# Performance work log

Measured on AMD Instinct MI355X. Metric: run time of the kernel, lower is better.

The kernel has to match this reference:

```python
import jax, jax.numpy as jnp
import numpy as np

HIDDEN = 64
EF_DIM = 3
RBOUND = 10.0
GROUP = 5
NEXP_MEAN = 0.05   # fixed normalization constants of the 'nexpnorm' RBF
NEXP_STD = 0.15
COORDS_WEIGHT = 1.0
N_NODES = 100000
N_GRAPHS = N_NODES // GROUP


def act(x):
    return jax.nn.relu(x)


def rbf(dist, num_rbf):
    # ExpNormal smearing with cosine cutoff (non-trainable), then fixed normalization.
    # dist: (..., 1) -> (..., num_rbf)
    alpha = 5.0 / RBOUND
    start = float(np.exp(-RBOUND))
    means = jnp.linspace(start, 1.0, num_rbf).astype(dist.dtype)
    beta = (2.0 / num_rbf * (1.0 - start)) ** -2
    cutoff = 0.5 * (jnp.cos(dist * jnp.pi / RBOUND) + 1.0) * (dist <= RBOUND)
    r = cutoff * jnp.exp(-beta * (jnp.exp(-alpha * dist) - means) ** 2)
    return (r - NEXP_MEAN) / NEXP_STD


def safe_pdist(a, b):
    # pairwise L2 norm (B,G,1,3)-(B,1,G,3) -> (B,G,G,1); grad-safe at zero
    d = a[:, :, None, :] - b[:, None, :, :]
    sq = jnp.sum(d * d, axis=-1, keepdims=True)
    return jnp.sqrt(jnp.where(sq == 0.0, 1.0, sq)) * (sq > 0.0)


def mlp2(x, w1, b1, w2, b2):
    return act(act(x @ w1 + b1) @ w2 + b2)


def mixed_wl(row, col, coord, vel, ic_wef, ic_pat, br_w1, br_b1, br_w2, br_b2, out_w, out_b):
    B = coord.shape[0] // GROUP
    c = coord.reshape(B, GROUP, 3)
    v = vel.reshape(B, GROUP, 3)
    mcd = safe_pdist(c, v)  # mixed coord-vel distances
    ef = jnp.concatenate([
        rbf(safe_pdist(c, c), EF_DIM),
        rbf(safe_pdist(v, v), EF_DIM),
        rbf(mcd, EF_DIM),
        rbf(jnp.swapaxes(mcd, 1, 2), EF_DIM),
    ], axis=-1)  # (B, 5, 5, 4*EF_DIM)
    # TwoFDisInit: linear embed * pattern embedding (diag tuples get pattern id 2, off-diag 1)
    idx = jnp.arange(GROUP)
    pattern = jnp.ones((GROUP, GROUP), dtype=jnp.int32).at[idx, idx].set(2)
    kemb = (ef @ ic_wef) * ic_pat[pattern]  # (B, 5, 5, H)
    # TwoFDisLayer (color_steps = 1): three branch MLPs, matrix-multiply mixing, residual add
    sm = mlp2(kemb, br_w1[0], br_b1[0], br_w2[0], br_b2[0])
    k0 = mlp2(kemb, br_w1[1], br_b1[1], br_w2[1], br_b2[1])
    k1 = mlp2(kemb, br_w1[2], br_b1[2], br_w2[2], br_b2[2])
    mult = jnp.einsum('bijd,bjkd->bikd', k0, k1)
    kemb = kemb + act((sm * mult) @ out_w + out_b)
    # gather per-edge tuple embedding
    return kemb[row // GROUP, row % GROUP, col % GROUP]  # (E, H)


def setup_inputs():
    key = jax.random.key(0)
    ks = jax.random.split(key, 20)
    N, H = N_NODES, HIDDEN
    # fully-connected (no self loops) edges inside each 5-node graph
    pairs = np.array([(i, j) for i in range(GROUP) for j in range(GROUP) if i != j])
    off = np.arange(N_GRAPHS) * GROUP
    row = (off[:, None] + pairs[None, :, 0]).reshape(-1)
    col = (off[:, None] + pairs[None, :, 1]).reshape(-1)
    edge_index = jnp.asarray(np.stack([row, col]), dtype=jnp.int32)
    g = lambda k, shp, s=0.05: jax.random.normal(k, shp, dtype=jnp.float32) * s
    return {
        'h': g(ks[0], (N, H), 0.5),
        'coord': g(ks[1], (N, 3), 1.0),
        'vel': g(ks[2], (N, 3), 1.0),
        'edge_index': edge_index,
        'e_w1': g(ks[3], (2 * H + 1 + H, H)), 'e_b1': jnp.zeros((H,), jnp.float32),
        'e_w2': g(ks[4], (H, H)), 'e_b2': jnp.zeros((H,), jnp.float32),
        'n_w1': g(ks[5], (2 * H, H)), 'n_b1': jnp.zeros((H,), jnp.float32),
        'n_w2': g(ks[6], (H, H)), 'n_b2': jnp.zeros((H,), jnp.float32),
        'c_w1': g(ks[7], (H, H)), 'c_b1': jnp.zeros((H,), jnp.float32),
        'c_w2': g(ks[8], (H, 1), 0.001),  # xavier gain=0.001, bias-free
        'v_w1': g(ks[9], (H, H)), 'v_b1': jnp.zeros((H,), jnp.float32),
        'v_w2': g(ks[10], (H, 1)), 'v_b2': jnp.zeros((1,), jnp.float32),
        'ic_wef': g(ks[11], (4 * EF_DIM, H), 0.1),
        'ic_pat': g(ks[12], (3, H), 0.1),
        'br_w1': g(ks[13], (3, H, H)), 'br_b1': jnp.zeros((3, H), jnp.float32),
        'br_w2': g(ks[14], (3, H, H)), 'br_b2': jnp.zeros((3, H), jnp.float32),
        'out_w': g(ks[15], (H, H)), 'out_b': jnp.zeros((H,), jnp.float32),
    }


def reference(h, coord, vel, edge_index, e_w1, e_b1, e_w2, e_b2, n_w1, n_b1, n_w2, n_b2,
              c_w1, c_b1, c_w2, v_w1, v_b1, v_w2, v_b2, ic_wef, ic_pat,
              br_w1, br_b1, br_w2, br_b2, out_w, out_b):
    row, col = edge_index[0], edge_index[1]
    N = h.shape[0]
    # coord2radial (norm_diff=False)
    coord_diff = coord[row] - coord[col]                      # (E, 3)
    radial = jnp.sum(coord_diff * coord_diff, axis=1, keepdims=True)  # (E, 1)
    # mixed 2-WL tuple embedding per edge
    kemb = mixed_wl(row, col, coord, vel, ic_wef, ic_pat, br_w1, br_b1, br_w2, br_b2, out_w, out_b)
    # edge model (attention=False)
    edge_feat = mlp2(jnp.concatenate([h[row], h[col], radial, kemb], axis=1),
                     e_w1, e_b1, e_w2, e_b2)                  # (E, H)
    # coord model: per-edge scalar (num_vectors_in=out=1), clamp, segment mean
    cmat = act(edge_feat @ c_w1 + c_b1) @ c_w2                # (E, 1)
    trans = jnp.clip(coord_diff * cmat, -100.0, 100.0)        # (E, 3)
    cnt = jax.ops.segment_sum(jnp.ones((row.shape[0],), trans.dtype), row, num_segments=N)
    agg = jax.ops.segment_sum(trans, row, num_segments=N) / jnp.maximum(cnt, 1.0)[:, None]
    # velocity update: coord += coord_mlp_vel(h) * vel
    vmat = act(h @ v_w1 + v_b1) @ v_w2 + v_b2                 # (N, 1)
    coord_out = (coord + agg * COORDS_WEIGHT + vel * vmat)[:, :, None]  # (N, 3, 1)
    # node model (recurrent=True)
    nagg = jax.ops.segment_sum(edge_feat, row, num_segments=N)
    h_out = h + (act(jnp.concatenate([h, nagg], axis=1) @ n_w1 + n_b1) @ n_w2 + n_b2)
    return h_out, coord_out
```

## Files before the change

### kernel.cpp

```cpp
#include <hip/hip_runtime.h>
#include <math.h>

#define HD 64
#define WPB 2

typedef unsigned short u16;
typedef unsigned int u32;
typedef __attribute__((ext_vector_type(8))) short short8;
typedef __attribute__((ext_vector_type(4))) float f32x4;

__device__ __forceinline__ u16 f2bf(float f) {
  u32 r;
  asm("v_cvt_pk_bf16_f32 %0, %1, %2" : "=v"(r) : "v"(f), "v"(f));
  return (u16)r;
}
__device__ __forceinline__ u32 pk2(float lo, float hi) {
  u32 r;
  asm("v_cvt_pk_bf16_f32 %0, %1, %2" : "=v"(r) : "v"(lo), "v"(hi));
  return r;
}
__device__ __forceinline__ float bf2f(u16 x) {
  return __uint_as_float(((u32)x) << 16);
}
__device__ __forceinline__ int uswz(int row, int col) {
  return (row << 6) | (col ^ (((row >> 2) & 3) << 4));
}
__device__ __forceinline__ float rlane(float v, int l) {
  return __uint_as_float(__builtin_amdgcn_readlane(__float_as_uint(v), l));
}
__device__ __forceinline__ void fence() {
  asm volatile("s_waitcnt lgkmcnt(0)" ::: "memory");
}

template <int MT, int RMAX>
__device__ __forceinline__ void loadA(const u16* A_, int t, short8* a0, short8* a1) {
  const int q8 = (t >> 4) << 3;
#pragma unroll
  for (int mt = 0; mt < MT; ++mt) {
    int row = mt * 16 + (t & 15);
    row = row > RMAX ? RMAX : row;
    const int idx = uswz(row, q8);
    a0[mt] = *reinterpret_cast<const short8*>(A_ + idx);
    a1[mt] = *reinterpret_cast<const short8*>(A_ + (idx ^ 32));
  }
}

template <int MTT>
__device__ __forceinline__ void mmh(const short8* a0, const short8* a1,
                                    const u16* __restrict__ WT, f32x4 (*acc)[2],
                                    int t, int nh) {
  const int c15 = t & 15;
  const int q8 = (t >> 4) << 3;
  short8 b[2][2];
#pragma unroll
  for (int n2 = 0; n2 < 2; ++n2) {
    const int nt = nh * 2 + n2;
#pragma unroll
    for (int s = 0; s < 2; ++s)
      b[n2][s] = *reinterpret_cast<const short8*>(WT + (nt * 16 + c15) * 64 + s * 32 + q8);
  }
#pragma unroll
  for (int mt = 0; mt < MTT; ++mt) {
#pragma unroll
    for (int n2 = 0; n2 < 2; ++n2)
      acc[mt][n2] = __builtin_amdgcn_mfma_f32_16x16x32_bf16(a0[mt], b[n2][0], acc[mt][n2], 0, 0, 0);
#pragma unroll
    for (int n2 = 0; n2 < 2; ++n2)
      acc[mt][n2] = __builtin_amdgcn_mfma_f32_16x16x32_bf16(a1[mt], b[n2][1], acc[mt][n2], 0, 0, 0);
  }
}

template <int MT, int RMAX, int EPI>
__device__ __forceinline__ void run_phase2(const u16* AA, const u16* AB,
                                           u16* DA, u16* DB,
                                           const u16* MA, const u16* MB,
                                           const u16* __restrict__ WT,
                                           const float* __restrict__ bias,
                                           const u16* __restrict__ PF,
                                           u32& pfa, int t, int rowoff = 0) {
  const int c15 = t & 15, q = t >> 4;
  constexpr int rowlim = (MT == 2) ? 25 : 5;
  const u32 pfv = reinterpret_cast<const u32*>(PF)[t * 32];
  short8 a0[2 * MT], a1[2 * MT];
  loadA<MT, RMAX>(AA, t, a0, a1);
  loadA<MT, RMAX>(AB, t, a0 + MT, a1 + MT);
#pragma unroll
  for (int nh = 0; nh < 2; ++nh) {
    f32x4 acc[2 * MT][2];
#pragma unroll
    for (int n2 = 0; n2 < 2; ++n2) {
      const int col = (nh * 2 + n2) * 16 + c15;
      const float bb = bias ? bias[col] : 0.0f;
#pragma unroll
      for (int mt = 0; mt < 2 * MT; ++mt) acc[mt][n2] = (f32x4){bb, bb, bb, bb};
    }
    mmh<2 * MT>(a0, a1, WT, acc, t, nh);
#pragma unroll
    for (int n2 = 0; n2 < 2; ++n2) {
      const int col = (nh * 2 + n2) * 16 + c15;
#pragma unroll
      for (int mt = 0; mt < 2 * MT; ++mt) {
        u16* D_ = (mt < MT) ? DA : DB;
        const u16* M_ = (mt < MT) ? MA : MB;
        const int r0 = (mt % MT) * 16 + q * 4;
        const int bix = uswz(r0 + rowoff, col);
#pragma unroll
        for (int i = 0; i < 4; ++i) {
          if (r0 + i < rowlim) {
            const int ix = bix + i * 64;
            float v = acc[mt][n2][i];
            if (EPI >= 2) v = fmaxf(v, 0.0f);
            if (EPI == 3) v *= bf2f(M_[ix]);
            if (EPI == 4) v += bf2f(D_[ix]);
            D_[ix] = f2bf(v);
          }
        }
      }
    }
  }
  pfa ^= pfv;
}

__global__ __launch_bounds__(256) void prepack(
    const float* __restrict__ br_w1, const float* __restrict__ br_w2,
    const float* __restrict__ out_w, const float* __restrict__ e_w1,
    const float* __restrict__ e_w2, const float* __restrict__ c_w1,
    const float* __restrict__ v_w1, const float* __restrict__ n_w1,
    const float* __restrict__ n_w2, const float* __restrict__ ic_wef,
    u16* __restrict__ W) {
  const int m = blockIdx.x;
  if (m == 16) {
    for (int e = threadIdx.x; e < 2048; e += blockDim.x) {
      const int n = e >> 5, k = e & 31;
      W[16 * 4096 + e] = (k < 12) ? f2bf(ic_wef[k * 64 + n]) : (u16)0;
    }
    return;
  }
  const float* src;
  switch (m) {
    case 0: src = br_w1; break;
    case 1: src = br_w1 + 4096; break;
    case 2: src = br_w1 + 8192; break;
    case 3: src = br_w2; break;
    case 4: src = br_w2 + 4096; break;
    case 5: src = br_w2 + 8192; break;
    case 6: src = out_w; break;
    case 7: src = e_w1; break;
    case 8: src = e_w1 + 64 * 64; break;
    case 9: src = e_w1 + 129 * 64; break;
    case 10: src = e_w2; break;
    case 11: src = c_w1; break;
    case 12: src = v_w1; break;
    case 13: src = n_w1; break;
    case 14: src = n_w1 + 64 * 64; break;
    default: src = n_w2; break;
  }
  u16* dst = W + m * 4096;
  for (int e = threadIdx.x; e < 4096; e += blockDim.x) {
    const int n = e >> 6, k = e & 63;
    dst[e] = f2bf(src[k * 64 + n]);
  }
}

__global__ __launch_bounds__(64 * WPB, 2) void egcl_mfma(
    const float* __restrict__ gh, const float* __restrict__ gcoord,
    const float* __restrict__ gvel, const u16* __restrict__ Wg,
    const float* __restrict__ e_w1, const float* __restrict__ e_b1,
    const float* __restrict__ e_b2,
    const float* __restrict__ n_b1, const float* __restrict__ n_b2,
    const float* __restrict__ c_b1, const float* __restrict__ c_w2,
    const float* __restrict__ v_b1, const float* __restrict__ v_w2,
    const float* __restrict__ v_b2,
    const float* __restrict__ ic_pat,
    const float* __restrict__ br_b1, const float* __restrict__ br_b2,
    const float* __restrict__ out_b,
    float* __restrict__ hout, float* __restrict__ cout, int B) {
  __shared__ __align__(16) u16 arena[WPB][9600];

  const int t = threadIdx.x & 63;
  const int wv = threadIdx.x >> 6;
  const int gA = (blockIdx.x * WPB + wv) * 2;
  if (gA >= B) return;
  int gB = gA + 1;
  if (gB >= B) gB = gA;

  u16* AR = arena[wv];
  u16* KA = AR;           u16* KB = AR + 1600;
  u16* TA = AR + 3200;    u16* TB = AR + 4800;
  u16* UA = AR + 6400;    u16* UB = AR + 8000;
  u16* EFa = TA;
  u16* EFb = TB;
  const int c15 = t & 15, q = t >> 4, q8 = q << 3;
  u32 pfa = 0;
#define WT(m) (Wg + (m) * 4096)

  short8 hA0, hA1;
  {
    int nd = c15 & 7;
    nd = nd > 4 ? 4 : nd;
    const int gg = (c15 & 8) ? gB : gA;
    const float* hp = gh + (size_t)(gg * 5 + nd) * HD + q8;
    const float4 f0 = *reinterpret_cast<const float4*>(hp);
    const float4 f1 = *reinterpret_cast<const float4*>(hp + 4);
    const float4 f2 = *reinterpret_cast<const float4*>(hp + 32);
    const float4 f3 = *reinterpret_cast<const float4*>(hp + 36);
    union { u32 w[4]; short8 s; } u0, u1;
    u0.w[0] = pk2(f0.x, f0.y); u0.w[1] = pk2(f0.z, f0.w);
    u0.w[2] = pk2(f1.x, f1.y); u0.w[3] = pk2(f1.z, f1.w);
    u1.w[0] = pk2(f2.x, f2.y); u1.w[1] = pk2(f2.z, f2.w);
    u1.w[2] = pk2(f3.x, f3.y); u1.w[3] = pk2(f3.z, f3.w);
    hA0 = u0.s;
    hA1 = u1.s;
  }

  float scvreg = 0.0f;
  if (t < 15) scvreg = gcoord[gA * 15 + t];
  else if (t >= 16 && t < 31) scvreg = gvel[gA * 15 + (t - 16)];
  else if (t >= 32 && t < 47) scvreg = gcoord[gB * 15 + (t - 32)];
  else if (t >= 48 && t < 63) scvreg = gvel[gB * 15 + (t - 48)];

#pragma unroll
  for (int z = 0; z < 8; ++z) {
    const int e = t + z * 64;
    if (e < 500) {
      const int gsel = e >= 250;
      const int ee = e - gsel * 250;
      const int row = ee / 10, cc = 12 + (ee % 10) * 2;
      *reinterpret_cast<u32*>((gsel ? EFb : EFa) + row * 32 + cc) = 0u;
    }
  }

  float sqcc = 0.0f;
  {
    const int lb = (t >= 32) ? 32 : 0;
    const int tt = t - lb;
    if (tt < 25) {
      u16* EF = lb ? EFb : EFa;
      const int ti = tt / 5, tj = tt % 5;
      const float cix = __shfl(scvreg, lb + ti * 3 + 0, 64), ciy = __shfl(scvreg, lb + ti * 3 + 1, 64), ciz = __shfl(scvreg, lb + ti * 3 + 2, 64);
      const float cjx = __shfl(scvreg, lb + tj * 3 + 0, 64), cjy = __shfl(scvreg, lb + tj * 3 + 1, 64), cjz = __shfl(scvreg, lb + tj * 3 + 2, 64);
      const float vix = __shfl(scvreg, lb + 16 + ti * 3 + 0, 64), viy = __shfl(scvreg, lb + 16 + ti * 3 + 1, 64), viz = __shfl(scvreg, lb + 16 + ti * 3 + 2, 64);
      const float vjx = __shfl(scvreg, lb + 16 + tj * 3 + 0, 64), vjy = __shfl(scvreg, lb + 16 + tj * 3 + 1, 64), vjz = __shfl(scvreg, lb + 16 + tj * 3 + 2, 64);
      {
        const float dx = cix - cjx, dy = ciy - cjy, dz = ciz - cjz;
        sqcc = dx * dx + dy * dy + dz * dz;
      }
      auto sd = [](float sq) { return (sq > 0.0f) ? sqrtf(sq) : 0.0f; };
      float sq2;
      const float dcc = sd(sqcc);
      {
        const float dx = vix - vjx, dy = viy - vjy, dz = viz - vjz;
        sq2 = dx * dx + dy * dy + dz * dz;
      }
      const float dvv = sd(sq2);
      {
        const float dx = cix - vjx, dy = ciy - vjy, dz = ciz - vjz;
        sq2 = dx * dx + dy * dy + dz * dz;
      }
      const float dcv = sd(sq2);
      {
        const float dx = cjx - vix, dy = cjy - viy, dz = cjz - viz;
        sq2 = dx * dx + dy * dy + dz * dz;
      }
      const float dvc = sd(sq2);
      auto rbf3 = [&](float d, int base) {
        const float cut = (d <= 10.0f) ? (0.5f * (cosf(d * 0.31415926535897931f) + 1.0f)) : 0.0f;
        const float e = expf(-0.5f * d);
        const float u0 = e - 4.5399929762484854e-05f;
        const float u1 = e - 0.50002270f;
        const float u2 = e - 1.0f;
        const float BETA = 2.2502043f;
        EF[tt * 32 + base + 0] = f2bf((cut * expf(-BETA * u0 * u0) - 0.05f) * (1.0f / 0.15f));
        EF[tt * 32 + base + 1] = f2bf((cut * expf(-BETA * u1 * u1) - 0.05f) * (1.0f / 0.15f));
        EF[tt * 32 + base + 2] = f2bf((cut * expf(-BETA * u2 * u2) - 0.05f) * (1.0f / 0.15f));
      };
      rbf3(dcc, 0);
      rbf3(dvv, 3);
      rbf3(dcv, 6);
      rbf3(dvc, 9);
    }
  }
  fence();

  {
    const u32 pfv = reinterpret_cast<const u32*>(WT(1))[t * 32];
    short8 aE[4];
#pragma unroll
    for (int gsel = 0; gsel < 2; ++gsel) {
      const u16* EF = gsel ? EFb : EFa;
#pragma unroll
      for (int mt = 0; mt < 2; ++mt) {
        int row = mt * 16 + c15;
        row = row > 24 ? 24 : row;
        aE[gsel * 2 + mt] = *reinterpret_cast<const short8*>(EF + row * 32 + q8);
      }
    }
    const u16* WTp = Wg + 16 * 4096;
#pragma unroll
    for (int nh = 0; nh < 2; ++nh) {
      f32x4 acc[4][2];
#pragma unroll
      for (int mt = 0; mt < 4; ++mt)
#pragma unroll
        for (int n2 = 0; n2 < 2; ++n2) acc[mt][n2] = (f32x4){0.f, 0.f, 0.f, 0.f};
      short8 b[2];
#pragma unroll
      for (int n2 = 0; n2 < 2; ++n2)
        b[n2] = *reinterpret_cast<const short8*>(WTp + ((nh * 2 + n2) * 16 + c15) * 32 + q8);
#pragma unroll
      for (int mt = 0; mt < 4; ++mt)
#pragma unroll
        for (int n2 = 0; n2 < 2; ++n2)
          acc[mt][n2] = __builtin_amdgcn_mfma_f32_16x16x32_bf16(aE[mt], b[n2], acc[mt][n2], 0, 0, 0);
#pragma unroll
      for (int n2 = 0; n2 < 2; ++n2) {
        const int col = (nh * 2 + n2) * 16 + c15;
        const float p1 = ic_pat[64 + col], p2 = ic_pat[128 + col];
#pragma unroll
        for (int mt = 0; mt < 4; ++mt) {
          u16* K_ = (mt < 2) ? KA : KB;
          const int r0 = (mt & 1) * 16 + q * 4;
          const int bix = uswz(r0, col);
#pragma unroll
          for (int i = 0; i < 4; ++i) {
            const int row = r0 + i;
            if (row < 25) {
              const bool diag = (row % 6) == 0;
              K_[bix + i * 64] = f2bf(acc[mt][n2][i] * (diag ? p2 : p1));
            }
          }
        }
      }
    }
    pfa ^= pfv;
  }
  fence();

  float svc[4][4];

  run_phase2<2, 24, 2>(KA, KB, TA, TB, nullptr, nullptr, WT(1), br_b1 + 64, WT(4), pfa, t); fence();
  run_phase2<2, 24, 2>(TA, TB, UA, UB, nullptr, nullptr, WT(4), br_b2 + 64, WT(2), pfa, t); fence();
  run_phase2<2, 24, 2>(KA, KB, TA, TB, nullptr, nullptr, WT(2), br_b1 + 128, WT(5), pfa, t); fence();
  run_phase2<2, 24, 2>(TA, TB, TA, TB, nullptr, nullptr, WT(5), br_b2 + 128, WT(0), pfa, t); fence();

  {
    float mu[2][25];
#pragma unroll
    for (int gsel = 0; gsel < 2; ++gsel)
#pragma unroll
      for (int p = 0; p < 25; ++p) mu[gsel][p] = 0.0f;
#pragma unroll
    for (int j = 0; j < 5; ++j) {
#pragma unroll
      for (int gsel = 0; gsel < 2; ++gsel) {
        const u16* Tg = gsel ? TB : TA;
        const u16* Ug = gsel ? UB : UA;
        float k1r[5], k0c[5];
#pragma unroll
        for (int k = 0; k < 5; ++k) k1r[k] = bf2f(Tg[uswz(j * 5 + k, t)]);
#pragma unroll
        for (int i = 0; i < 5; ++i) k0c[i] = bf2f(Ug[uswz(i * 5 + j, t)]);
#pragma unroll
        for (int i = 0; i < 5; ++i)
#pragma unroll
          for (int k = 0; k < 5; ++k)
            mu[gsel][i * 5 + k] = fmaf(k0c[i], k1r[k], mu[gsel][i * 5 + k]);
      }
    }
    fence();
#pragma unroll
    for (int p = 0; p < 25; ++p) {
      UA[uswz(p, t)] = f2bf(mu[0][p]);
      UB[uswz(p, t)] = f2bf(mu[1][p]);
    }
  }
  fence();

  run_phase2<2, 24, 2>(KA, KB, TA, TB, nullptr, nullptr, WT(0), br_b1, WT(3), pfa, t); fence();
  run_phase2<2, 24, 3>(TA, TB, TA, TB, UA, UB, WT(3), br_b2, WT(6), pfa, t); fence();
  run_phase2<2, 24, 4>(TA, TB, KA, KB, nullptr, nullptr, WT(6), out_b, WT(9), pfa, t); fence();
  run_phase2<2, 24, 1>(KA, KB, TA, TB, nullptr, nullptr, WT(9), nullptr, WT(7), pfa, t); fence();

  float svv[4];
  {
    const u32 pfv = reinterpret_cast<const u32*>(WT(8))[t * 32];
    float s[4] = {0.f, 0.f, 0.f, 0.f};
#pragma unroll
    for (int nh = 0; nh < 2; ++nh) {
      f32x4 aA[1][2], aB[1][2], aV[1][2];
#pragma unroll
      for (int n2 = 0; n2 < 2; ++n2) {
        const float bv = v_b1[(nh * 2 + n2) * 16 + c15];
        aA[0][n2] = (f32x4){0.f, 0.f, 0.f, 0.f};
        aB[0][n2] = (f32x4){0.f, 0.f, 0.f, 0.f};
        aV[0][n2] = (f32x4){bv, bv, bv, bv};
      }
      mmh<1>(&hA0, &hA1, WT(7), aA, t, nh);
      mmh<1>(&hA0, &hA1, WT(8), aB, t, nh);
      mmh<1>(&hA0, &hA1, WT(12), aV, t, nh);
#pragma unroll
      for (int n2 = 0; n2 < 2; ++n2) {
        const int col = (nh * 2 + n2) * 16 + c15;
        const float w2v = v_w2[col];
#pragma unroll
        for (int i = 0; i < 4; ++i) {
          const int r = q * 4 + i;
          if (r < 5) {
            UA[uswz(r, col)] = f2bf(aA[0][n2][i]);
            UA[uswz(r + 8, col)] = f2bf(aB[0][n2][i]);
          } else if (r >= 8 && r < 13) {
            UB[uswz(r - 8, col)] = f2bf(aA[0][n2][i]);
            UB[uswz(r, col)] = f2bf(aB[0][n2][i]);
          }
          s[i] += fmaxf(aV[0][n2][i], 0.0f) * w2v;
        }
      }
    }
#pragma unroll
    for (int i = 0; i < 4; ++i) {
      float ss = s[i];
      ss += __shfl_xor(ss, 1, 64);
      ss += __shfl_xor(ss, 2, 64);
      ss += __shfl_xor(ss, 4, 64);
      ss += __shfl_xor(ss, 8, 64);
      svv[i] = ss;
    }
    pfa ^= pfv;
  }
  fence();

  {
    float ec[2][20];
#pragma unroll
    for (int gsel = 0; gsel < 2; ++gsel) {
      const int lb = gsel * 32;
      const u16* Ug = gsel ? UB : UA;
      const u16* Tg = gsel ? TB : TA;
      float aAc[5], aBc[5];
#pragma unroll
      for (int i = 0; i < 5; ++i) {
        aAc[i] = bf2f(Ug[uswz(i, t)]);
        aBc[i] = bf2f(Ug[uswz(8 + i, t)]);
      }
      const float eb1v = e_b1[t];
      const float wradv = e_w1[128 * HD + t];
#pragma unroll
      for (int p = 0; p < 20; ++p) {
        const int i = p >> 2, jj = p & 3;
        const int j = jj + (jj >= i ? 1 : 0);
        const float radial = rlane(sqcc, lb + i * 5 + j);
        const float cc = bf2f(Tg[uswz(i * 5 + j, t)]);
        ec[gsel][p] = fmaxf(aAc[i] + aBc[j] + radial * wradv + cc + eb1v, 0.0f);
      }
    }
    fence();
#pragma unroll
    for (int p = 0; p < 20; ++p) {
      TA[uswz(p, t)] = f2bf(ec[0][p]);
      TB[uswz(p, t)] = f2bf(ec[1][p]);
    }
  }
  fence();

  run_phase2<2, 24, 2>(TA, TB, UA, UB, nullptr, nullptr, WT(10), e_b2, WT(11), pfa, t); fence();

#pragma unroll
  for (int gsel = 0; gsel < 2; ++gsel) {
    const u16* Ug = gsel ? UB : UA;
#pragma unroll
    for (int i = 0; i < 5; ++i) {
      float na = 0.0f;
#pragma unroll
      for (int jj = 0; jj < 4; ++jj) na += bf2f(Ug[uswz(4 * i + jj, t)]);
      KA[uswz(gsel * 8 + i, t)] = f2bf(na);
    }
  }
  fence();

  {
    const u32 pfv = reinterpret_cast<const u32*>(WT(13))[t * 32];
    short8 a0[4], a1[4];
    loadA<2, 24>(UA, t, a0, a1);
    loadA<2, 24>(UB, t, a0 + 2, a1 + 2);
    float s[4][4];
#pragma unroll
    for (int mt = 0; mt < 4; ++mt)
#pragma unroll
      for (int i = 0; i < 4; ++i) s[mt][i] = 0.0f;
#pragma unroll
    for (int nh = 0; nh < 2; ++nh) {
      f32x4 acc[4][2];
#pragma unroll
      for (int n2 = 0; n2 < 2; ++n2) {
        const float bv = c_b1[(nh * 2 + n2) * 16 + c15];
#pragma unroll
        for (int mt = 0; mt < 4; ++mt) acc[mt][n2] = (f32x4){bv, bv, bv, bv};
      }
      mmh<4>(a0, a1, WT(11), acc, t, nh);
#pragma unroll
      for (int n2 = 0; n2 < 2; ++n2) {
        const int col = (nh * 2 + n2) * 16 + c15;
        const float w2v = c_w2[col];
#pragma unroll
        for (int mt = 0; mt < 4; ++mt)
#pragma unroll
          for (int i = 0; i < 4; ++i)
            s[mt][i] += fmaxf(acc[mt][n2][i], 0.0f) * w2v;
      }
    }
#pragma unroll
    for (int mt = 0; mt < 4; ++mt)
#pragma unroll
      for (int i = 0; i < 4; ++i) {
        float ss = s[mt][i];
        ss += __shfl_xor(ss, 1, 64);
        ss += __shfl_xor(ss, 2, 64);
        ss += __shfl_xor(ss, 4, 64);
        ss += __shfl_xor(ss, 8, 64);
        svc[mt][i] = ss;
      }
    pfa ^= pfv;
  }

  {
    const float vb2 = v_b2[0];
    float coutreg = 0.0f;
#pragma unroll
    for (int gsel = 0; gsel < 2; ++gsel) {
      const int lb = gsel * 32;
#pragma unroll
      for (int i = 0; i < 5; ++i) {
        const int rr = gsel * 8 + i;
        const float vmi = rlane(svv[rr & 3], (rr >> 2) << 4) + vb2;
#pragma unroll
        for (int dd = 0; dd < 3; ++dd) {
          const float ci = rlane(scvreg, lb + i * 3 + dd);
          float s = 0.0f;
#pragma unroll
          for (int jj = 0; jj < 4; ++jj) {
            const int j = jj + (jj >= i ? 1 : 0);
            const int p = i * 4 + jj;
            const float cmp = rlane(svc[gsel * 2 + (p >> 4)][p & 3], ((p & 15) >> 2) << 4);
            float tr = (ci - rlane(scvreg, lb + j * 3 + dd)) * cmp;
            tr = fminf(fmaxf(tr, -100.0f), 100.0f);
            s += tr;
          }
          const float val = ci + 0.25f * s + rlane(scvreg, lb + 16 + i * 3 + dd) * vmi;
          if (t == lb + i * 3 + dd) coutreg = val;
        }
      }
    }
    if (t < 15) cout[gA * 15 + t] = coutreg;
    else if (t >= 32 && t < 47) cout[gB * 15 + (t - 32)] = coutreg;
  }

  {
    const u32 pfv = reinterpret_cast<const u32*>(WT(15))[t * 32];
    short8 a0k[1], a1k[1];
    loadA<1, 15>(KA, t, a0k, a1k);
#pragma unroll
    for (int nh = 0; nh < 2; ++nh) {
      f32x4 acc[1][2];
#pragma unroll
      for (int n2 = 0; n2 < 2; ++n2) {
        const float nb = n_b1[(nh * 2 + n2) * 16 + c15];
        acc[0][n2] = (f32x4){nb, nb, nb, nb};
      }
      mmh<1>(&hA0, &hA1, WT(13), acc, t, nh);
      mmh<1>(a0k, a1k, WT(14), acc, t, nh);
#pragma unroll
      for (int n2 = 0; n2 < 2; ++n2) {
        const int col = (nh * 2 + n2) * 16 + c15;
#pragma unroll
        for (int i = 0; i < 4; ++i) {
          const int r = q * 4 + i;
          if (r < 5 || (r >= 8 && r < 13))
            TA[uswz(r, col)] = f2bf(fmaxf(acc[0][n2][i], 0.0f));
        }
      }
    }
    pfa ^= pfv;
  }
  fence();

  {
    short8 a0[1], a1[1];
    loadA<1, 15>(TA, t, a0, a1);
#pragma unroll
    for (int nh = 0; nh < 2; ++nh) {
      f32x4 acc[1][2];
#pragma unroll
      for (int n2 = 0; n2 < 2; ++n2) {
        const float nb = n_b2[(nh * 2 + n2) * 16 + c15];
        acc[0][n2] = (f32x4){nb, nb, nb, nb};
      }
      mmh<1>(a0, a1, WT(15), acc, t, nh);
#pragma unroll
      for (int n2 = 0; n2 < 2; ++n2) {
        const int col = (nh * 2 + n2) * 16 + c15;
#pragma unroll
        for (int i = 0; i < 4; ++i) {
          const int r = q * 4 + i;
          if (r < 5) {
            const size_t ix = (size_t)(gA * 5 + r) * HD + col;
            hout[ix] = gh[ix] + acc[0][n2][i];
          } else if (r >= 8 && r < 13) {
            const size_t ix = (size_t)(gB * 5 + (r - 8)) * HD + col;
            hout[ix] = gh[ix] + acc[0][n2][i];
          }
        }
      }
    }
  }

  if (B == -7) cout[1] = __uint_as_float(pfa);
#undef WT
}

extern "C" void kernel_launch(void* const* d_in, const int* in_sizes, int n_in,
                              void* d_out, int out_size, void* d_ws, size_t ws_size,
                              hipStream_t stream) {
  if (n_in < 27) return;
  const float* gh    = (const float*)d_in[0];
  const float* coord = (const float*)d_in[1];
  const float* vel   = (const float*)d_in[2];
  const float* e_w1 = (const float*)d_in[4];
  const float* e_b1 = (const float*)d_in[5];
  const float* e_w2 = (const float*)d_in[6];
  const float* e_b2 = (const float*)d_in[7];
  const float* n_w1 = (const float*)d_in[8];
  const float* n_b1 = (const float*)d_in[9];
  const float* n_w2 = (const float*)d_in[10];
  const float* n_b2 = (const float*)d_in[11];
  const float* c_w1 = (const float*)d_in[12];
  const float* c_b1 = (const float*)d_in[13];
  const float* c_w2 = (const float*)d_in[14];
  const float* v_w1 = (const float*)d_in[15];
  const float* v_b1 = (const float*)d_in[16];
  const float* v_w2 = (const float*)d_in[17];
  const float* v_b2 = (const float*)d_in[18];
  const float* ic_wef = (const float*)d_in[19];
  const float* ic_pat = (const float*)d_in[20];
  const float* br_w1 = (const float*)d_in[21];
  const float* br_b1 = (const float*)d_in[22];
  const float* br_w2 = (const float*)d_in[23];
  const float* br_b2 = (const float*)d_in[24];
  const float* out_w = (const float*)d_in[25];
  const float* out_b = (const float*)d_in[26];

  const int N = in_sizes[0] / HD;
  const int B = N / 5;
  float* hout = (float*)d_out;
  float* cout = (float*)d_out + (size_t)N * HD;
  u16* W = (u16*)d_ws;

  prepack<<<17, 256, 0, stream>>>(br_w1, br_w2, out_w, e_w1, e_w2, c_w1, v_w1,
                                  n_w1, n_w2, ic_wef, W);

  const int gpb = WPB * 2;
  const int blocks = (B + gpb - 1) / gpb;
  egcl_mfma<<<blocks, 64 * WPB, 0, stream>>>(
      gh, coord, vel, W, e_w1, e_b1, e_b2, n_b1, n_b2, c_b1, c_w2, v_b1, v_w2,
      v_b2, ic_pat, br_b1, br_b2, out_b, hout, cout, B);
}
```

Baseline: 246.0 us.

## Fuse branch MLP phases, drop weight prefetch, merge edge/node GEMMs

```diff
diff --git a/kernel.cpp b/kernel.cpp
--- a/kernel.cpp
+++ b/kernel.cpp
@@ -76,11 +76,9 @@
                                            const u16* MA, const u16* MB,
                                            const u16* __restrict__ WT,
                                            const float* __restrict__ bias,
-                                           const u16* __restrict__ PF,
-                                           u32& pfa, int t, int rowoff = 0) {
+                                           int t, int rowoff = 0) {
   const int c15 = t & 15, q = t >> 4;
   constexpr int rowlim = (MT == 2) ? 25 : 5;
-  const u32 pfv = reinterpret_cast<const u32*>(PF)[t * 32];
   short8 a0[2 * MT], a1[2 * MT];
   loadA<MT, RMAX>(AA, t, a0, a1);
   loadA<MT, RMAX>(AB, t, a0 + MT, a1 + MT);
@@ -118,7 +116,6 @@
       }
     }
   }
-  pfa ^= pfv;
 }
 
 __global__ __launch_bounds__(256) void prepack(
@@ -191,7 +188,6 @@
   u16* EFa = TA;
   u16* EFb = TB;
   const int c15 = t & 15, q = t >> 4, q8 = q << 3;
-  u32 pfa = 0;
 #define WT(m) (Wg + (m) * 4096)
 
   short8 hA0, hA1;
@@ -283,7 +279,6 @@
   fence();
 
   {
-    const u32 pfv = reinterpret_cast<const u32*>(WT(1))[t * 32];
     short8 aE[4];
 #pragma unroll
     for (int gsel = 0; gsel < 2; ++gsel) {
@@ -332,16 +327,92 @@
         }
       }
     }
-    pfa ^= pfv;
-  }
-  fence();
-
-  float svc[4][4];
-
-  run_phase2<2, 24, 2>(KA, KB, TA, TB, nullptr, nullptr, WT(1), br_b1 + 64, WT(4), pfa, t); fence();
-  run_phase2<2, 24, 2>(TA, TB, UA, UB, nullptr, nullptr, WT(4), br_b2 + 64, WT(2), pfa, t); fence();
-  run_phase2<2, 24, 2>(KA, KB, TA, TB, nullptr, nullptr, WT(2), br_b1 + 128, WT(5), pfa, t); fence();
-  run_phase2<2, 24, 2>(TA, TB, TA, TB, nullptr, nullptr, WT(5), br_b2 + 128, WT(0), pfa, t); fence();
+  }
+  fence();
+
+  {
+    short8 a0[4], a1[4];
+    loadA<2, 24>(KA, t, a0, a1);
+    loadA<2, 24>(KB, t, a0 + 2, a1 + 2);
+#pragma unroll
+    for (int nh = 0; nh < 2; ++nh) {
+      f32x4 ac0[4][2], ac1[4][2];
+#pragma unroll
+      for (int n2 = 0; n2 < 2; ++n2) {
+        const int col = (nh * 2 + n2) * 16 + c15;
+        const float b0 = br_b1[64 + col], b1 = br_b1[128 + col];
+#pragma unroll
+        for (int mt = 0; mt < 4; ++mt) {
+          ac0[mt][n2] = (f32x4){b0, b0, b0, b0};
+          ac1[mt][n2] = (f32x4){b1, b1, b1, b1};
+        }
+      }
+      mmh<4>(a0, a1, WT(1), ac0, t, nh);
+      mmh<4>(a0, a1, WT(2), ac1, t, nh);
+#pragma unroll
+      for (int n2 = 0; n2 < 2; ++n2) {
+        const int col = (nh * 2 + n2) * 16 + c15;
+#pragma unroll
+        for (int mt = 0; mt < 4; ++mt) {
+          u16* T_ = (mt < 2) ? TA : TB;
+          u16* U_ = (mt < 2) ? UA : UB;
+          const int r0 = (mt & 1) * 16 + q * 4;
+          const int bix = uswz(r0, col);
+#pragma unroll
+          for (int i = 0; i < 4; ++i) {
+            if (r0 + i < 25) {
+              T_[bix + i * 64] = f2bf(fmaxf(ac0[mt][n2][i], 0.0f));
+              U_[bix + i * 64] = f2bf(fmaxf(ac1[mt][n2][i], 0.0f));
+            }
+          }
+        }
+      }
+    }
+  }
+  fence();
+
+  {
+    short8 a0[4], a1[4], c0[4], c1[4];
+    loadA<2, 24>(TA, t, a0, a1);
+    loadA<2, 24>(TB, t, a0 + 2, a1 + 2);
+    loadA<2, 24>(UA, t, c0, c1);
+    loadA<2, 24>(UB, t, c0 + 2, c1 + 2);
+#pragma unroll
+    for (int nh = 0; nh < 2; ++nh) {
+      f32x4 ac0[4][2], ac1[4][2];
+#pragma unroll
+      for (int n2 = 0; n2 < 2; ++n2) {
+        const int col = (nh * 2 + n2) * 16 + c15;
+        const float b0 = br_b2[64 + col], b1 = br_b2[128 + col];
+#pragma unroll
+        for (int mt = 0; mt < 4; ++mt) {
+          ac0[mt][n2] = (f32x4){b0, b0, b0, b0};
+          ac1[mt][n2] = (f32x4){b1, b1, b1, b1};
+        }
+      }
+      mmh<4>(a0, a1, WT(4), ac0, t, nh);
+      mmh<4>(c0, c1, WT(5), ac1, t, nh);
+#pragma unroll
+      for (int n2 = 0; n2 < 2; ++n2) {
+        const int col = (nh * 2 + n2) * 16 + c15;
+#pragma unroll
+        for (int mt = 0; mt < 4; ++mt) {
+          u16* T_ = (mt < 2) ? TA : TB;
+          u16* U_ = (mt < 2) ? UA : UB;
+          const int r0 = (mt & 1) * 16 + q * 4;
+          const int bix = uswz(r0, col);
+#pragma unroll
+          for (int i = 0; i < 4; ++i) {
+            if (r0 + i < 25) {
+              T_[bix + i * 64] = f2bf(fmaxf(ac0[mt][n2][i], 0.0f));
+              U_[bix + i * 64] = f2bf(fmaxf(ac1[mt][n2][i], 0.0f));
+            }
+          }
+        }
+      }
+    }
+  }
+  fence();
 
   {
     float mu[2][25];
@@ -357,9 +428,9 @@
         const u16* Ug = gsel ? UB : UA;
         float k1r[5], k0c[5];
 #pragma unroll
-        for (int k = 0; k < 5; ++k) k1r[k] = bf2f(Tg[uswz(j * 5 + k, t)]);
-#pragma unroll
-        for (int i = 0; i < 5; ++i) k0c[i] = bf2f(Ug[uswz(i * 5 + j, t)]);
+        for (int k = 0; k < 5; ++k) k1r[k] = bf2f(Ug[uswz(j * 5 + k, t)]);
+#pragma unroll
+        for (int i = 0; i < 5; ++i) k0c[i] = bf2f(Tg[uswz(i * 5 + j, t)]);
 #pragma unroll
         for (int i = 0; i < 5; ++i)
 #pragma unroll
@@ -376,25 +447,29 @@
   }
   fence();
 
-  run_phase2<2, 24, 2>(KA, KB, TA, TB, nullptr, nullptr, WT(0), br_b1, WT(3), pfa, t); fence();
-  run_phase2<2, 24, 3>(TA, TB, TA, TB, UA, UB, WT(3), br_b2, WT(6), pfa, t); fence();
-  run_phase2<2, 24, 4>(TA, TB, KA, KB, nullptr, nullptr, WT(6), out_b, WT(9), pfa, t); fence();
-  run_phase2<2, 24, 1>(KA, KB, TA, TB, nullptr, nullptr, WT(9), nullptr, WT(7), pfa, t); fence();
+  run_phase2<2, 24, 2>(KA, KB, TA, TB, nullptr, nullptr, WT(0), br_b1, t); fence();
+  run_phase2<2, 24, 3>(TA, TB, TA, TB, UA, UB, WT(3), br_b2, t); fence();
+  run_phase2<2, 24, 4>(TA, TB, KA, KB, nullptr, nullptr, WT(6), out_b, t); fence();
 
   float svv[4];
   {
-    const u32 pfv = reinterpret_cast<const u32*>(WT(8))[t * 32];
+    short8 a0[4], a1[4];
+    loadA<2, 24>(KA, t, a0, a1);
+    loadA<2, 24>(KB, t, a0 + 2, a1 + 2);
     float s[4] = {0.f, 0.f, 0.f, 0.f};
 #pragma unroll
     for (int nh = 0; nh < 2; ++nh) {
-      f32x4 aA[1][2], aB[1][2], aV[1][2];
+      f32x4 accC[4][2], aA[1][2], aB[1][2], aV[1][2];
 #pragma unroll
       for (int n2 = 0; n2 < 2; ++n2) {
         const float bv = v_b1[(nh * 2 + n2) * 16 + c15];
+#pragma unroll
+        for (int mt = 0; mt < 4; ++mt) accC[mt][n2] = (f32x4){0.f, 0.f, 0.f, 0.f};
         aA[0][n2] = (f32x4){0.f, 0.f, 0.f, 0.f};
         aB[0][n2] = (f32x4){0.f, 0.f, 0.f, 0.f};
         aV[0][n2] = (f32x4){bv, bv, bv, bv};
       }
+      mmh<4>(a0, a1, WT(9), accC, t, nh);
       mmh<1>(&hA0, &hA1, WT(7), aA, t, nh);
       mmh<1>(&hA0, &hA1, WT(8), aB, t, nh);
       mmh<1>(&hA0, &hA1, WT(12), aV, t, nh);
@@ -402,6 +477,15 @@
       for (int n2 = 0; n2 < 2; ++n2) {
         const int col = (nh * 2 + n2) * 16 + c15;
         const float w2v = v_w2[col];
+#pragma unroll
+        for (int mt = 0; mt < 4; ++mt) {
+          u16* T_ = (mt < 2) ? TA : TB;
+          const int r0 = (mt & 1) * 16 + q * 4;
+          const int bix = uswz(r0, col);
+#pragma unroll
+          for (int i = 0; i < 4; ++i)
+            if (r0 + i < 25) T_[bix + i * 64] = f2bf(accC[mt][n2][i]);
+        }
 #pragma unroll
         for (int i = 0; i < 4; ++i) {
           const int r = q * 4 + i;
@@ -425,7 +509,6 @@
       ss += __shfl_xor(ss, 8, 64);
       svv[i] = ss;
     }
-    pfa ^= pfv;
   }
   fence();
 
@@ -462,41 +545,73 @@
   }
   fence();
 
-  run_phase2<2, 24, 2>(TA, TB, UA, UB, nullptr, nullptr, WT(10), e_b2, WT(11), pfa, t); fence();
-
-#pragma unroll
-  for (int gsel = 0; gsel < 2; ++gsel) {
-    const u16* Ug = gsel ? UB : UA;
-#pragma unroll
-    for (int i = 0; i < 5; ++i) {
-      float na = 0.0f;
-#pragma unroll
-      for (int jj = 0; jj < 4; ++jj) na += bf2f(Ug[uswz(4 * i + jj, t)]);
-      KA[uswz(gsel * 8 + i, t)] = f2bf(na);
-    }
-  }
-  fence();
-
-  {
-    const u32 pfv = reinterpret_cast<const u32*>(WT(13))[t * 32];
+  {
     short8 a0[4], a1[4];
-    loadA<2, 24>(UA, t, a0, a1);
-    loadA<2, 24>(UB, t, a0 + 2, a1 + 2);
-    float s[4][4];
-#pragma unroll
-    for (int mt = 0; mt < 4; ++mt)
-#pragma unroll
-      for (int i = 0; i < 4; ++i) s[mt][i] = 0.0f;
+    loadA<2, 24>(TA, t, a0, a1);
+    loadA<2, 24>(TB, t, a0 + 2, a1 + 2);
 #pragma unroll
     for (int nh = 0; nh < 2; ++nh) {
       f32x4 acc[4][2];
 #pragma unroll
       for (int n2 = 0; n2 < 2; ++n2) {
-        const float bv = c_b1[(nh * 2 + n2) * 16 + c15];
-#pragma unroll
-        for (int mt = 0; mt < 4; ++mt) acc[mt][n2] = (f32x4){bv, bv, bv, bv};
-      }
-      mmh<4>(a0, a1, WT(11), acc, t, nh);
+        const float bb = e_b2[(nh * 2 + n2) * 16 + c15];
+#pragma unroll
+        for (int mt = 0; mt < 4; ++mt) acc[mt][n2] = (f32x4){bb, bb, bb, bb};
+      }
+      mmh<4>(a0, a1, WT(10), acc, t, nh);
+#pragma unroll
+      for (int n2 = 0; n2 < 2; ++n2) {
+        const int col = (nh * 2 + n2) * 16 + c15;
+#pragma unroll
+        for (int mt = 0; mt < 4; ++mt) {
+          u16* U_ = (mt < 2) ? UA : UB;
+          const int gsel = mt >> 1;
+          const int r0 = (mt & 1) * 16 + q * 4;
+          const int bix = uswz(r0, col);
+          float na = 0.0f;
+#pragma unroll
+          for (int i = 0; i < 4; ++i) {
+            const float v = fmaxf(acc[mt][n2][i], 0.0f);
+            if (r0 + i < 25) U_[bix + i * 64] = f2bf(v);
+            na += v;
+          }
+          if (!(mt & 1)) {
+            KA[uswz(gsel * 8 + q, col)] = f2bf(na);
+          } else if (q == 0) {
+            KA[uswz(gsel * 8 + 4, col)] = f2bf(na);
+          }
+        }
+      }
+    }
+  }
+  fence();
+
+  float svc[4][4];
+  {
+    short8 u0[4], u1[4], k0[1], k1[1];
+    loadA<2, 24>(UA, t, u0, u1);
+    loadA<2, 24>(UB, t, u0 + 2, u1 + 2);
+    loadA<1, 15>(KA, t, k0, k1);
+    float s[4][4];
+#pragma unroll
+    for (int mt = 0; mt < 4; ++mt)
+#pragma unroll
+      for (int i = 0; i < 4; ++i) s[mt][i] = 0.0f;
+#pragma unroll
+    for (int nh = 0; nh < 2; ++nh) {
+      f32x4 accc[4][2], accn[1][2];
+#pragma unroll
+      for (int n2 = 0; n2 < 2; ++n2) {
+        const int col = (nh * 2 + n2) * 16 + c15;
+        const float bv = c_b1[col];
+        const float nb = n_b1[col];
+#pragma unroll
+        for (int mt = 0; mt < 4; ++mt) accc[mt][n2] = (f32x4){bv, bv, bv, bv};
+        accn[0][n2] = (f32x4){nb, nb, nb, nb};
+      }
+      mmh<4>(u0, u1, WT(11), accc, t, nh);
+      mmh<1>(&hA0, &hA1, WT(13), accn, t, nh);
+      mmh<1>(k0, k1, WT(14), accn, t, nh);
 #pragma unroll
       for (int n2 = 0; n2 < 2; ++n2) {
         const int col = (nh * 2 + n2) * 16 + c15;
@@ -505,7 +620,13 @@
         for (int mt = 0; mt < 4; ++mt)
 #pragma unroll
           for (int i = 0; i < 4; ++i)
-            s[mt][i] += fmaxf(acc[mt][n2][i], 0.0f) * w2v;
+            s[mt][i] += fmaxf(accc[mt][n2][i], 0.0f) * w2v;
+#pragma unroll
+        for (int i = 0; i < 4; ++i) {
+          const int r = q * 4 + i;
+          if (r < 5 || (r >= 8 && r < 13))
+            TA[uswz(r, col)] = f2bf(fmaxf(accn[0][n2][i], 0.0f));
+        }
       }
     }
 #pragma unroll
@@ -519,8 +640,8 @@
         ss += __shfl_xor(ss, 8, 64);
         svc[mt][i] = ss;
       }
-    pfa ^= pfv;
-  }
+  }
+  fence();
 
   {
     const float vb2 = v_b2[0];
@@ -553,35 +674,6 @@
     if (t < 15) cout[gA * 15 + t] = coutreg;
     else if (t >= 32 && t < 47) cout[gB * 15 + (t - 32)] = coutreg;
   }
-
-  {
-    const u32 pfv = reinterpret_cast<const u32*>(WT(15))[t * 32];
-    short8 a0k[1], a1k[1];
-    loadA<1, 15>(KA, t, a0k, a1k);
-#pragma unroll
-    for (int nh = 0; nh < 2; ++nh) {
-      f32x4 acc[1][2];
-#pragma unroll
-      for (int n2 = 0; n2 < 2; ++n2) {
-        const float nb = n_b1[(nh * 2 + n2) * 16 + c15];
-        acc[0][n2] = (f32x4){nb, nb, nb, nb};
-      }
-      mmh<1>(&hA0, &hA1, WT(13), acc, t, nh);
-      mmh<1>(a0k, a1k, WT(14), acc, t, nh);
-#pragma unroll
-      for (int n2 = 0; n2 < 2; ++n2) {
-        const int col = (nh * 2 + n2) * 16 + c15;
-#pragma unroll
-        for (int i = 0; i < 4; ++i) {
-          const int r = q * 4 + i;
-          if (r < 5 || (r >= 8 && r < 13))
-            TA[uswz(r, col)] = f2bf(fmaxf(acc[0][n2][i], 0.0f));
-        }
-      }
-    }
-    pfa ^= pfv;
-  }
-  fence();
 
   {
     short8 a0[1], a1[1];
@@ -612,8 +704,6 @@
       }
     }
   }
-
-  if (B == -7) cout[1] = __uint_as_float(pfa);
 #undef WT
 }
 
```

Measured after the change: 237.4 us. -3.5%, faster.
